# Optimization experiments

Measured on AMD Instinct MI355X. Metric: run time of the kernel, lower is better.

The kernel has to match this reference:

```python
import jax, jax.numpy as jnp
import numpy as np

N_NODES = 100000


def gcn_conv(x, edge_index, edge_weight, W, b):
    # PyG GCNConv: x' = D^{-1/2} (A + I) D^{-1/2} (x W) + b
    n = x.shape[0]
    h = x @ W  # [N, out]
    src, dst = edge_index[0], edge_index[1]
    loop = jnp.arange(n, dtype=edge_index.dtype)
    src2 = jnp.concatenate([src, loop])
    dst2 = jnp.concatenate([dst, loop])
    ew2 = jnp.concatenate([edge_weight, jnp.ones((n,), dtype=x.dtype)])
    deg = jax.ops.segment_sum(ew2, dst2, num_segments=n)  # weighted in-degree incl self-loop
    dinv = jnp.where(deg > 0, jax.lax.rsqrt(deg), 0.0)
    norm = dinv[src2] * ew2 * dinv[dst2]  # [E+N]
    msgs = h[src2] * norm[:, None]  # gather + scale
    out = jax.ops.segment_sum(msgs, dst2, num_segments=n)  # scatter-add at targets
    return out + b


def setup_inputs() -> dict:
    key = jax.random.key(0)
    k1, k2, k3, k4, k5 = jax.random.split(key, 5)
    F_in, H, C = 128, 64, 16
    E = 1600000
    x = jax.random.normal(k1, (N_NODES, F_in), dtype=jnp.float32)
    edge_index = jax.random.randint(k2, (2, E), 0, N_NODES, dtype=jnp.int64)
    edge_weights = jax.random.uniform(k3, (E,), dtype=jnp.float32)
    W1 = jax.random.normal(k4, (F_in, H), dtype=jnp.float32) * (1.0 / np.sqrt(F_in))
    b1 = jnp.zeros((H,), dtype=jnp.float32)
    W2 = jax.random.normal(k5, (H, C), dtype=jnp.float32) * (1.0 / np.sqrt(H))
    b2 = jnp.zeros((C,), dtype=jnp.float32)
    return {"x": x, "edge_index": edge_index, "edge_weights": edge_weights,
            "W1": W1, "b1": b1, "W2": W2, "b2": b2}


def reference(x, edge_index, edge_weights, W1, b1, W2, b2):
    h = gcn_conv(x, edge_index, edge_weights, W1, b1)
    h = jax.nn.relu(h)
    # dropout inactive at inference (F.dropout with training=False is identity)
    h = gcn_conv(h, edge_index, edge_weights, W2, b2)
    return jax.nn.log_softmax(h, axis=1)
```

## Files before the change

### kernel.cpp

```cpp
#include <hip/hip_runtime.h>


#define BSHIFT 7
#define BNODES 128
#define NBUK_MAX 1024
#define CSTR 16
#define CAP 3072
#define CHUNK 4096
#define EPB 16

typedef unsigned short ushort_t;
typedef unsigned int uint_t;
typedef unsigned short us4 __attribute__((ext_vector_type(4)));

__device__ inline ushort_t f2bf(float f) {
    uint_t u = __float_as_uint(f);
    return (ushort_t)((u + 0x7FFF + ((u >> 16) & 1)) >> 16);
}
__device__ inline float bf2f(ushort_t b) {
    return __uint_as_float(((uint_t)b) << 16);
}

__global__ __launch_bounds__(1024) void k_binit(int* __restrict__ bcur, int nbuk) {
    int t = threadIdx.x;
    if (t < nbuk) bcur[t * CSTR] = t * CAP;
}

__global__ __launch_bounds__(256) void k_p1(const int* __restrict__ src,
                                            const int* __restrict__ dst,
                                            const float* __restrict__ ew,
                                            int* __restrict__ bcur,
                                            int2* __restrict__ tmp, int E, int nbuk) {
    __shared__ int lcnt[NBUK_MAX];
    __shared__ int lbase[NBUK_MAX];
    const int t = threadIdx.x;
    const int base = blockIdx.x * CHUNK;
    for (int j = t; j < nbuk; j += 256) lcnt[j] = 0;
    __syncthreads();
    int d_r[EPB];
#pragma unroll
    for (int k = 0; k < EPB; ++k) {
        int e = base + k * 256 + t;
        int d = (e < E) ? dst[e] : -1;
        d_r[k] = d;
        if (d >= 0) atomicAdd(&lcnt[d >> BSHIFT], 1);
    }
    __syncthreads();
    for (int j = t; j < nbuk; j += 256) {
        int c = lcnt[j];
        lbase[j] = c ? atomicAdd(&bcur[j * CSTR], c) : 0;
        lcnt[j] = 0;
    }
    __syncthreads();
#pragma unroll
    for (int k = 0; k < EPB; ++k) {
        int d = d_r[k];
        if (d < 0) continue;
        int e = base + k * 256 + t;
        int b = d >> BSHIFT;
        int p = lbase[b] + atomicAdd(&lcnt[b], 1);
        if (p >= nbuk * CAP) continue;
        int2 pk;
        pk.x = src[e] | ((d & (BNODES - 1)) << 17);
        pk.y = __float_as_int(ew[e]);
        tmp[p] = pk;
    }
}

__global__ __launch_bounds__(1024) void k_pscan(const int* __restrict__ bcur,
                                                int* __restrict__ boff, int nbuk) {
    __shared__ int lds[1024];
    const int t = threadIdx.x;
    int v = (t < nbuk) ? (bcur[t * CSTR] - t * CAP) : 0;
    lds[t] = v;
    __syncthreads();
    for (int off = 1; off < 1024; off <<= 1) {
        int u = (t >= off) ? lds[t - off] : 0;
        __syncthreads();
        lds[t] += u;
        __syncthreads();
    }
    if (t < nbuk) boff[t] = lds[t] - v;
    if (t == nbuk - 1) boff[nbuk] = lds[t];
}

__global__ __launch_bounds__(256) void k_p2(const int2* __restrict__ tmp,
                                            const int* __restrict__ bcur,
                                            const int* __restrict__ boff,
                                            int* __restrict__ rowptr,
                                            int2* __restrict__ epack,
                                            float* __restrict__ dinv,
                                            int n, int nbuk) {
    __shared__ int cnt[BNODES];
    __shared__ int pos[BNODES];
    __shared__ float degf[BNODES];
    const int b = blockIdx.x, t = threadIdx.x;
    const int node0 = b << BSHIFT;
    if (t < BNODES) { cnt[t] = 0; degf[t] = 0.f; }
    __syncthreads();
    const int lo_t = b * CAP, hi_t = bcur[b * CSTR];
    const int outb = boff[b];
    for (int i = lo_t + t; i < hi_t; i += 256) {
        int2 pk = tmp[i];
        int dlo = (pk.x >> 17) & (BNODES - 1);
        atomicAdd(&cnt[dlo], 1);
        atomicAdd(&degf[dlo], __int_as_float(pk.y));
    }
    __syncthreads();
    int own = (t < BNODES) ? cnt[t] : 0;
    if (t < BNODES) pos[t] = own;
    __syncthreads();
    for (int off = 1; off < BNODES; off <<= 1) {
        int u = (t < BNODES && t >= off) ? pos[t - off] : 0;
        __syncthreads();
        if (t < BNODES) pos[t] += u;
        __syncthreads();
    }
    if (t < BNODES) {
        int excl = pos[t] - own;
        int node = node0 + t;
        if (node < n) {
            rowptr[node] = outb + excl;
            dinv[node] = rsqrtf(1.0f + degf[t]);
        }
        pos[t] = excl;
    }
    if (b == nbuk - 1 && t == 0) rowptr[n] = outb + (hi_t - lo_t);
    __syncthreads();
    for (int i = lo_t + t; i < hi_t; i += 256) {
        int2 pk = tmp[i];
        int dlo = (pk.x >> 17) & (BNODES - 1);
        int p = outb + atomicAdd(&pos[dlo], 1);
        int2 o;
        o.x = pk.x & 0x1FFFF;
        o.y = pk.y;
        epack[p] = o;
    }
}

__global__ __launch_bounds__(256) void k_gemm1(const float* __restrict__ x,
                                               const float* __restrict__ W,
                                               const float* __restrict__ dinv,
                                               ushort_t* __restrict__ h, int n) {
    __shared__ float Ws[128 * 64];
    __shared__ float xs[16][128];
    const int t = threadIdx.x;
    for (int i = t; i < 128 * 64; i += 256) Ws[i] = W[i];
    const int node0 = blockIdx.x * 16;
    for (int i = t; i < 16 * 128; i += 256) {
        int nn = i >> 7, kk = i & 127;
        int node = node0 + nn;
        xs[nn][kk] = (node < n) ? x[(size_t)node * 128 + kk] : 0.0f;
    }
    __syncthreads();
    const int fg = t & 15;
    const int ng = t >> 4;
    const float4* Ws4 = (const float4*)Ws;
    float4 acc = {0.f, 0.f, 0.f, 0.f};
#pragma unroll 8
    for (int k = 0; k < 128; ++k) {
        float4 w = Ws4[k * 16 + fg];
        float xv = xs[ng][k];
        acc.x = fmaf(xv, w.x, acc.x);
        acc.y = fmaf(xv, w.y, acc.y);
        acc.z = fmaf(xv, w.z, acc.z);
        acc.w = fmaf(xv, w.w, acc.w);
    }
    const int node = node0 + ng;
    if (node < n) {
        float di = dinv[node];
        us4 pk;
        pk.x = f2bf(acc.x * di);
        pk.y = f2bf(acc.y * di);
        pk.z = f2bf(acc.z * di);
        pk.w = f2bf(acc.w * di);
        *(us4*)(h + (size_t)node * 64 + fg * 4) = pk;
    }
}

__global__ __launch_bounds__(256) void k_agg64(const ushort_t* __restrict__ h,
                                               const int* __restrict__ rowptr,
                                               const int2* __restrict__ ep,
                                               const float* __restrict__ dinv,
                                               float* __restrict__ agg, int n) {
    const int node = __builtin_amdgcn_readfirstlane((int)((blockIdx.x * 256 + threadIdx.x) >> 6));
    const int lane = threadIdx.x & 63;
    if (node >= n) return;
    const float di = dinv[node];
    const int lo = rowptr[node], hi = rowptr[node + 1];
    const ushort_t* __restrict__ hl = h + lane;
    float accE = 0.f;
    int i = lo;
    if (i + 8 <= hi) {
        int2 pb[8], nb[8];
#pragma unroll
        for (int k = 0; k < 8; ++k) pb[k] = ep[i + k];
        i += 8;
        for (; i + 8 <= hi; i += 8) {
#pragma unroll
            for (int k = 0; k < 8; ++k) nb[k] = ep[i + k];
            float v[8];
#pragma unroll
            for (int k = 0; k < 8; ++k) v[k] = bf2f(hl[(size_t)pb[k].x * 64]);
#pragma unroll
            for (int k = 0; k < 8; ++k) accE = fmaf(v[k], __int_as_float(pb[k].y), accE);
#pragma unroll
            for (int k = 0; k < 8; ++k) pb[k] = nb[k];
        }
        {
            float v[8];
#pragma unroll
            for (int k = 0; k < 8; ++k) v[k] = bf2f(hl[(size_t)pb[k].x * 64]);
#pragma unroll
            for (int k = 0; k < 8; ++k) accE = fmaf(v[k], __int_as_float(pb[k].y), accE);
        }
    }
    for (; i < hi; ++i) {
        int2 p = ep[i];
        accE = fmaf(bf2f(hl[(size_t)p.x * 64]), __int_as_float(p.y), accE);
    }
    float self = bf2f(hl[(size_t)node * 64]);
    agg[(size_t)node * 64 + lane] = di * (accE + self);
}

__global__ __launch_bounds__(256) void k_agg16(const ushort_t* __restrict__ h,
                                               const int* __restrict__ rowptr,
                                               const int2* __restrict__ ep,
                                               const float* __restrict__ dinv,
                                               float* __restrict__ agg, int n) {
    const int node = (blockIdx.x * 256 + threadIdx.x) >> 4;
    const int lane = threadIdx.x & 15;
    if (node >= n) return;
    const float di = dinv[node];
    float accE = 0.f;
    const int lo = rowptr[node], hi = rowptr[node + 1];
    int i = lo;
    for (; i + 3 < hi; i += 4) {
        int2 p0 = ep[i], p1 = ep[i + 1], p2 = ep[i + 2], p3 = ep[i + 3];
        float v0 = bf2f(h[(size_t)p0.x * 16 + lane]);
        float v1 = bf2f(h[(size_t)p1.x * 16 + lane]);
        float v2 = bf2f(h[(size_t)p2.x * 16 + lane]);
        float v3 = bf2f(h[(size_t)p3.x * 16 + lane]);
        accE = fmaf(v0, __int_as_float(p0.y), accE);
        accE = fmaf(v1, __int_as_float(p1.y), accE);
        accE = fmaf(v2, __int_as_float(p2.y), accE);
        accE = fmaf(v3, __int_as_float(p3.y), accE);
    }
    for (; i < hi; ++i) {
        int2 p = ep[i];
        accE = fmaf(bf2f(h[(size_t)p.x * 16 + lane]), __int_as_float(p.y), accE);
    }
    float self = bf2f(h[(size_t)node * 16 + lane]);
    agg[(size_t)node * 16 + lane] = di * (accE + self);
}

__global__ __launch_bounds__(256) void k_gemm2(const float* __restrict__ a,
                                               const float* __restrict__ W,
                                               const float* __restrict__ b1,
                                               const float* __restrict__ dinv,
                                               ushort_t* __restrict__ h2, int n) {
    __shared__ float Ws[64 * 16];
    __shared__ float xs[32][68];
    const int t = threadIdx.x;
    for (int i = t; i < 64 * 16; i += 256) Ws[i] = W[i];
    const int node0 = blockIdx.x * 32;
    for (int i = t; i < 32 * 64; i += 256) {
        int nn = i >> 6, kk = i & 63;
        int node = node0 + nn;
        xs[nn][kk] = (node < n) ? fmaxf(a[(size_t)node * 64 + kk] + b1[kk], 0.0f) : 0.0f;
    }
    __syncthreads();
    const int f = t & 15;
    const int ng = t >> 4;
    float a0 = 0.f, a1 = 0.f;
#pragma unroll 4
    for (int k = 0; k < 64; ++k) {
        float wv = Ws[k * 16 + f];
        a0 = fmaf(xs[ng][k], wv, a0);
        a1 = fmaf(xs[ng + 16][k], wv, a1);
    }
    if (node0 + ng < n)
        h2[(size_t)(node0 + ng) * 16 + f] = f2bf(a0 * dinv[node0 + ng]);
    if (node0 + ng + 16 < n)
        h2[(size_t)(node0 + ng + 16) * 16 + f] = f2bf(a1 * dinv[node0 + ng + 16]);
}

__global__ void k_logsoftmax(float* __restrict__ out, const float* __restrict__ b2, int n) {
    int i = blockIdx.x * blockDim.x + threadIdx.x;
    if (i >= n) return;
    const size_t base = (size_t)i * 16;
    float v[16];
#pragma unroll
    for (int f = 0; f < 16; ++f) v[f] = out[base + f] + b2[f];
    float m = v[0];
#pragma unroll
    for (int f = 1; f < 16; ++f) m = fmaxf(m, v[f]);
    float s = 0.f;
#pragma unroll
    for (int f = 0; f < 16; ++f) s += __expf(v[f] - m);
    float lse = __logf(s);
#pragma unroll
    for (int f = 0; f < 16; ++f) out[base + f] = v[f] - m - lse;
}

extern "C" void kernel_launch(void* const* d_in, const int* in_sizes, int n_in,
                              void* d_out, int out_size, void* d_ws, size_t ws_size,
                              hipStream_t stream) {
    const float* x  = (const float*)d_in[0];
    const int*   ei = (const int*)d_in[1];
    const float* ew = (const float*)d_in[2];
    const float* W1 = (const float*)d_in[3];
    const float* b1 = (const float*)d_in[4];
    const float* W2 = (const float*)d_in[5];
    const float* b2 = (const float*)d_in[6];
    float* out = (float*)d_out;

    const int n = in_sizes[0] / 128;
    const int E = in_sizes[2];
    const int* srcv = ei;
    const int* dstv = ei + E;
    const int nbuk = (n + BNODES - 1) >> BSHIFT;

    float* wsf = (float*)d_ws;
    size_t off = 0;
    float* dinv = wsf + off; off += n;
    ushort_t* h1b = (ushort_t*)(wsf + off); off += (size_t)n * 32;
    float* agg1 = wsf + off; off += (size_t)n * 64;
    off = (off + 1) & ~(size_t)1;
    int2* epack = (int2*)(wsf + off); off += (size_t)E * 2;
    int* rowptr = (int*)(wsf + off); off += n + 1;
    int* boff_d = (int*)(wsf + off); off += NBUK_MAX + 1;
    int* bcur   = (int*)(wsf + off); off += (size_t)NBUK_MAX * CSTR;
    int2* tmp   = (int2*)agg1;

    const int TB = 256;

    k_binit<<<1, 1024, 0, stream>>>(bcur, nbuk);
    k_p1<<<(E + CHUNK - 1) / CHUNK, TB, 0, stream>>>(srcv, dstv, ew, bcur, tmp, E, nbuk);
    k_pscan<<<1, 1024, 0, stream>>>(bcur, boff_d, nbuk);
    k_p2<<<nbuk, TB, 0, stream>>>(tmp, bcur, boff_d, rowptr, epack, dinv, n, nbuk);

    k_gemm1<<<(n + 15) / 16, TB, 0, stream>>>(x, W1, dinv, h1b, n);
    k_agg64<<<(n * 64 + TB - 1) / TB, TB, 0, stream>>>(h1b, rowptr, epack, dinv, agg1, n);

    k_gemm2<<<(n + 31) / 32, TB, 0, stream>>>(agg1, W2, b1, dinv, h1b, n);
    k_agg16<<<(n * 16 + TB - 1) / TB, TB, 0, stream>>>(h1b, rowptr, epack, dinv, out, n);

    k_logsoftmax<<<(n + TB - 1) / TB, TB, 0, stream>>>(out, b2, n);
}
```

Baseline: 316.9 us.

## Register-block gemm1 over four nodes per thread with float4 x loads

The first-layer GEMM now processes 64 nodes per block instead of 16. Each thread accumulates four nodes, so every W float4 read from shared memory is reused four times. x is staged in two K-halves with float4 global loads into a padded shared tile. This cuts the W1 shared-memory reload per node and the shared-memory traffic per FMA, at the cost of more registers and fewer blocks.

```diff
diff --git a/kernel.cpp b/kernel.cpp
--- a/kernel.cpp
+++ b/kernel.cpp
@@ -143,38 +143,70 @@
                                                const float* __restrict__ dinv,
                                                ushort_t* __restrict__ h, int n) {
     __shared__ float Ws[128 * 64];
-    __shared__ float xs[16][128];
+    __shared__ float xs[64][68];
     const int t = threadIdx.x;
     for (int i = t; i < 128 * 64; i += 256) Ws[i] = W[i];
-    const int node0 = blockIdx.x * 16;
-    for (int i = t; i < 16 * 128; i += 256) {
-        int nn = i >> 7, kk = i & 127;
-        int node = node0 + nn;
-        xs[nn][kk] = (node < n) ? x[(size_t)node * 128 + kk] : 0.0f;
-    }
-    __syncthreads();
+    const int node0 = blockIdx.x * 64;
     const int fg = t & 15;
     const int ng = t >> 4;
+    float4 acc[4];
+#pragma unroll
+    for (int j = 0; j < 4; ++j) acc[j] = make_float4(0.f, 0.f, 0.f, 0.f);
     const float4* Ws4 = (const float4*)Ws;
-    float4 acc = {0.f, 0.f, 0.f, 0.f};
-#pragma unroll 8
-    for (int k = 0; k < 128; ++k) {
-        float4 w = Ws4[k * 16 + fg];
-        float xv = xs[ng][k];
-        acc.x = fmaf(xv, w.x, acc.x);
-        acc.y = fmaf(xv, w.y, acc.y);
-        acc.z = fmaf(xv, w.z, acc.z);
-        acc.w = fmaf(xv, w.w, acc.w);
-    }
-    const int node = node0 + ng;
-    if (node < n) {
-        float di = dinv[node];
-        us4 pk;
-        pk.x = f2bf(acc.x * di);
-        pk.y = f2bf(acc.y * di);
-        pk.z = f2bf(acc.z * di);
-        pk.w = f2bf(acc.w * di);
-        *(us4*)(h + (size_t)node * 64 + fg * 4) = pk;
+    for (int half = 0; half < 2; ++half) {
+        __syncthreads();
+        for (int i = t; i < 64 * 16; i += 256) {
+            int nn = i >> 4, q = i & 15;
+            int node = node0 + nn;
+            float4 v = (node < n) ? ((const float4*)x)[(size_t)node * 32 + half * 16 + q]
+                                  : make_float4(0.f, 0.f, 0.f, 0.f);
+            *(float4*)&xs[nn][q * 4] = v;
+        }
+        __syncthreads();
+#pragma unroll 4
+        for (int kb = 0; kb < 16; ++kb) {
+            float4 xv[4];
+#pragma unroll
+            for (int j = 0; j < 4; ++j)
+                xv[j] = *(const float4*)&xs[ng + 16 * j][kb * 4];
+            const int kg = half * 64 + kb * 4;
+            float4 w0 = Ws4[(kg + 0) * 16 + fg];
+            float4 w1 = Ws4[(kg + 1) * 16 + fg];
+            float4 w2 = Ws4[(kg + 2) * 16 + fg];
+            float4 w3 = Ws4[(kg + 3) * 16 + fg];
+#pragma unroll
+            for (int j = 0; j < 4; ++j) {
+                acc[j].x = fmaf(xv[j].x, w0.x, acc[j].x);
+                acc[j].y = fmaf(xv[j].x, w0.y, acc[j].y);
+                acc[j].z = fmaf(xv[j].x, w0.z, acc[j].z);
+                acc[j].w = fmaf(xv[j].x, w0.w, acc[j].w);
+                acc[j].x = fmaf(xv[j].y, w1.x, acc[j].x);
+                acc[j].y = fmaf(xv[j].y, w1.y, acc[j].y);
+                acc[j].z = fmaf(xv[j].y, w1.z, acc[j].z);
+                acc[j].w = fmaf(xv[j].y, w1.w, acc[j].w);
+                acc[j].x = fmaf(xv[j].z, w2.x, acc[j].x);
+                acc[j].y = fmaf(xv[j].z, w2.y, acc[j].y);
+                acc[j].z = fmaf(xv[j].z, w2.z, acc[j].z);
+                acc[j].w = fmaf(xv[j].z, w2.w, acc[j].w);
+                acc[j].x = fmaf(xv[j].w, w3.x, acc[j].x);
+                acc[j].y = fmaf(xv[j].w, w3.y, acc[j].y);
+                acc[j].z = fmaf(xv[j].w, w3.z, acc[j].z);
+                acc[j].w = fmaf(xv[j].w, w3.w, acc[j].w);
+            }
+        }
+    }
+#pragma unroll
+    for (int j = 0; j < 4; ++j) {
+        int node = node0 + ng + 16 * j;
+        if (node < n) {
+            float di = dinv[node];
+            us4 pk;
+            pk.x = f2bf(acc[j].x * di);
+            pk.y = f2bf(acc[j].y * di);
+            pk.z = f2bf(acc[j].z * di);
+            pk.w = f2bf(acc[j].w * di);
+            *(us4*)(h + (size_t)node * 64 + fg * 4) = pk;
+        }
     }
 }
 
@@ -340,7 +372,7 @@
     k_pscan<<<1, 1024, 0, stream>>>(bcur, boff_d, nbuk);
     k_p2<<<nbuk, TB, 0, stream>>>(tmp, bcur, boff_d, rowptr, epack, dinv, n, nbuk);
 
-    k_gemm1<<<(n + 15) / 16, TB, 0, stream>>>(x, W1, dinv, h1b, n);
+    k_gemm1<<<(n + 63) / 64, TB, 0, stream>>>(x, W1, dinv, h1b, n);
     k_agg64<<<(n * 64 + TB - 1) / TB, TB, 0, stream>>>(h1b, rowptr, epack, dinv, agg1, n);
 
     k_gemm2<<<(n + 31) / 32, TB, 0, stream>>>(agg1, W2, b1, dinv, h1b, n);
```

Result: faster. 299.7 us (-5.5%).
